# Performance work log

Hardware: AMD Instinct MI355X
Metric: run time of the kernel (lower is better)

Reference implementation:

```python
import jax, jax.numpy as jnp
import numpy as np

ORDER = 4


def setup_inputs() -> dict:
    key = jax.random.key(0)
    k1, k2, k3, k4 = jax.random.split(key, 4)
    B, IN, OUT = 8192, 1024, 1024
    x = jax.random.normal(k1, (B, IN), dtype=jnp.float32)
    base_weight = jax.random.normal(k2, (OUT, IN), dtype=jnp.float32) * (1.0 / np.sqrt(IN))
    std = 1.0 / (IN * np.sqrt(ORDER))
    taylor_coeffs = jax.random.normal(k3, (OUT, IN, ORDER), dtype=jnp.float32) * std
    bound = 1.0 / np.sqrt(IN)
    bias = jax.random.uniform(k4, (OUT,), dtype=jnp.float32, minval=-bound, maxval=bound)
    return {"x": x, "base_weight": base_weight, "taylor_coeffs": taylor_coeffs, "bias": bias}


def reference(x, base_weight, taylor_coeffs, bias):
    # base path: SiLU(x) @ W^T
    base_out = jnp.einsum('bi,oi->bo', jax.nn.silu(x), base_weight)
    # taylor path: x_powers[b,i,k] = x**k, k=0..ORDER-1; contract with coeffs[o,i,k]
    powers = jnp.arange(ORDER, dtype=x.dtype)  # [K]
    x_powers = x[:, :, None] ** powers  # [B, IN, K]
    taylor_out = jnp.einsum('bik,oik->bo', x_powers, taylor_coeffs)
    return base_out + taylor_out + bias
```

## Files before the change

kernel.cpp:

```cpp
#include <hip/hip_runtime.h>
#include <hip/hip_bf16.h>

#define GLOBAL_AS __attribute__((address_space(1)))
#define LDS_AS    __attribute__((address_space(3)))

typedef __bf16 bf16x8 __attribute__((ext_vector_type(8)));
typedef float  f32x4  __attribute__((ext_vector_type(4)));

constexpr int BATCH = 8192;
constexpr int IN    = 1024;
constexpr int OUT   = 1024;
constexpr int KDIM  = IN * 4;
constexpr int BM = 128, BN = 256, BK = 64;
constexpr int NKT  = KDIM / BK;
constexpr int LDSBUF = 24576;

__device__ __forceinline__ unsigned short f2bf(float f) {
    union { float f; unsigned u; } v; v.f = f;
    unsigned r = v.u + 0x7fffu + ((v.u >> 16) & 1u);
    return (unsigned short)(r >> 16);
}
__device__ __forceinline__ unsigned pk(unsigned short a, unsigned short b) {
    return (unsigned)a | ((unsigned)b << 16);
}

__global__ __launch_bounds__(256) void prep_b(const float* __restrict__ W,
                                              const float* __restrict__ C,
                                              const float* __restrict__ bias,
                                              unsigned short* __restrict__ Bb,
                                              float* __restrict__ be) {
    const int o = blockIdx.x, t = threadIdx.x;
    const int i0 = t * 4;
    const float4* c4 = reinterpret_cast<const float4*>(C + ((size_t)o * IN + i0) * 4);
    float4 w4 = *reinterpret_cast<const float4*>(W + (size_t)o * IN + i0);
    float wv[4] = {w4.x, w4.y, w4.z, w4.w};
    float s = 0.f;
    unsigned d[8];
#pragma unroll
    for (int j = 0; j < 4; ++j) {
        float4 c = c4[j];
        s += c.x;
        d[2*j]   = pk(f2bf(wv[j]), f2bf(c.y));
        d[2*j+1] = pk(f2bf(c.z),   f2bf(c.w));
    }
    uint4* dst = reinterpret_cast<uint4*>(Bb + (size_t)o * KDIM + i0 * 4);
    dst[0] = make_uint4(d[0], d[1], d[2], d[3]);
    dst[1] = make_uint4(d[4], d[5], d[6], d[7]);
#pragma unroll
    for (int off = 32; off > 0; off >>= 1) s += __shfl_down(s, off, 64);
    __shared__ float red[4];
    if ((t & 63) == 0) red[t >> 6] = s;
    __syncthreads();
    if (t == 0) be[o] = bias[o] + red[0] + red[1] + red[2] + red[3];
}

__global__ __launch_bounds__(512, 2) void gemm_kan(
        const float* __restrict__ x,
        const unsigned short* __restrict__ Bb,
        const float* __restrict__ be,
        float* __restrict__ out) {
    extern __shared__ unsigned short smem[];

    const int t    = threadIdx.x;
    const int l    = blockIdx.x;
    const int bm   = l & 63;
    const int bn   = l >> 6;
    const int lane = t & 63;
    const int wave = t >> 6;
    const int wr   = wave >> 2;
    const int wc   = wave & 3;
    const int l15  = lane & 15;
    const int quad = lane >> 4;
    const int x7   = l15 & 7;

    const unsigned short* bP[4];
#pragma unroll
    for (int i = 0; i < 4; ++i) {
        int ch = i * 512 + t, r = ch >> 3, g = (ch & 7) ^ (r & 7);
        bP[i] = Bb + (size_t)(bn * BN + r) * KDIM + g * 8;
    }

    const int arow  = t >> 2;
    const int axi   = t & 3;
    const int aoff0 = arow * 64 + (((axi * 2)     ^ (arow & 7)) * 8);
    const int aoff1 = arow * 64 + (((axi * 2 + 1) ^ (arow & 7)) * 8);
    const float4* xp = reinterpret_cast<const float4*>(
        x + (size_t)(bm * BM + arow) * IN + axi * 4);

    const int aRd = (wr * 32 + l15) * 64;
    const int bRd = 8192 + (wc * 64 + l15) * 64;

    f32x4 acc[4][4];
    const f32x4 zero = {0.f, 0.f, 0.f, 0.f};
#pragma unroll
    for (int i = 0; i < 4; ++i)
#pragma unroll
        for (int j = 0; j < 4; ++j) acc[i][j] = zero;

#define STAGE_B(tile, buf) do {                                                        \
    _Pragma("unroll")                                                                  \
    for (int i_ = 0; i_ < 4; ++i_)                                                     \
        __builtin_amdgcn_global_load_lds(                                              \
            (const GLOBAL_AS void*)(bP[i_] + (size_t)(tile) * BK),                     \
            (LDS_AS void*)(smem + (buf) * LDSBUF + 8192 + (i_ * 512 + t) * 8),         \
            16, 0, 0);                                                                 \
} while (0)

#define STAGE_A(buf, v) do {                                                           \
    float e_[4] = {(v).x, (v).y, (v).z, (v).w};                                        \
    unsigned d_[8];                                                                    \
    _Pragma("unroll")                                                                  \
    for (int j = 0; j < 4; ++j) {                                                      \
        float xv_ = e_[j];                                                             \
        float m_  = xv_ * -1.44269504088896f;                          \
        float ex_, r_;                                                                 \
        asm("v_exp_f32 %0, %1" : "=v"(ex_) : "v"(m_));                 \
        float a_  = 1.0f + ex_;                                                        \
        asm("v_rcp_f32 %0, %1" : "=v"(r_) : "v"(a_));                                  \
        float s_  = xv_ * r_;                                                          \
        float x2_ = xv_ * xv_;                                                         \
        float x3_ = x2_ * xv_;                                                         \
        asm("v_cvt_pk_bf16_f32 %0, %1, %2" : "=v"(d_[2*j])   : "v"(s_),  "v"(xv_));    \
        asm("v_cvt_pk_bf16_f32 %0, %1, %2" : "=v"(d_[2*j+1]) : "v"(x2_), "v"(x3_));    \
    }                                                                                  \
    unsigned short* ab_ = smem + (buf) * LDSBUF;                                       \
    *reinterpret_cast<uint4*>(ab_ + aoff0) = make_uint4(d_[0], d_[1], d_[2], d_[3]);   \
    *reinterpret_cast<uint4*>(ab_ + aoff1) = make_uint4(d_[4], d_[5], d_[6], d_[7]);   \
} while (0)

    float4 xa   = xp[0];
    float4 xb   = xp[4];
    float4 xcur = xp[8];
    float4 xnext = xcur;
    STAGE_B(0, 0);
    STAGE_B(1, 1);
    STAGE_A(0, xa);
    STAGE_A(1, xb);
    asm volatile("s_waitcnt vmcnt(4) lgkmcnt(0)" ::: "memory");
    __builtin_amdgcn_s_barrier();

    int cb = 0;
    for (int kt = 0; kt < NKT; ++kt) {
        const unsigned short* sb = smem + cb * LDSBUF;
        const int nb = (cb >= 1) ? cb - 1 : 2;

        if (kt + 3 < NKT) xnext = xp[(kt + 3) * 4];
        if (kt + 2 < NKT) STAGE_B(kt + 2, nb);

#pragma unroll
        for (int kk = 0; kk < 2; ++kk) {
            const int ck = ((kk * 4 + quad) ^ x7) * 8;
            bf16x8 af[4], bv[4];
            af[0] = *reinterpret_cast<const bf16x8*>(sb + aRd + ck);
            af[1] = *reinterpret_cast<const bf16x8*>(sb + aRd + 1024 + ck);
            af[2] = *reinterpret_cast<const bf16x8*>(sb + aRd + 4096 + ck);
            af[3] = *reinterpret_cast<const bf16x8*>(sb + aRd + 5120 + ck);
#pragma unroll
            for (int ni = 0; ni < 4; ++ni)
                bv[ni] = *reinterpret_cast<const bf16x8*>(sb + bRd + ni * 1024 + ck);
#pragma unroll
            for (int mi = 0; mi < 4; ++mi)
#pragma unroll
                for (int ni = 0; ni < 4; ++ni)
                    acc[mi][ni] = __builtin_amdgcn_mfma_f32_16x16x32_bf16(
                        af[mi], bv[ni], acc[mi][ni], 0, 0, 0);
        }

        if (kt + 2 < NKT) {
            STAGE_A(nb, xcur);
            xcur = xnext;
        }

        if (kt < NKT - 3) {
            asm volatile("s_waitcnt vmcnt(5) lgkmcnt(0)" ::: "memory");
            __builtin_amdgcn_s_barrier();
        } else if (kt == NKT - 3) {
            asm volatile("s_waitcnt vmcnt(4) lgkmcnt(0)" ::: "memory");
            __builtin_amdgcn_s_barrier();
        } else if (kt == NKT - 2) {
            asm volatile("s_waitcnt vmcnt(0) lgkmcnt(0)" ::: "memory");
            __builtin_amdgcn_s_barrier();
        }
        cb = (cb == 2) ? 0 : cb + 1;
    }

#undef STAGE_A
#undef STAGE_B

    float bev[4];
#pragma unroll
    for (int ni = 0; ni < 4; ++ni)
        bev[ni] = be[bn * BN + wc * 64 + ni * 16 + l15];

#pragma unroll
    for (int mg = 0; mg < 4; ++mg) {
        const int grow = bm * BM + (mg >> 1) * 64 + wr * 32 + (mg & 1) * 16 + quad * 4;
#pragma unroll
        for (int ni = 0; ni < 4; ++ni) {
            const int gcol = bn * BN + wc * 64 + ni * 16 + l15;
            float* po = out + (size_t)grow * OUT + gcol;
#pragma unroll
            for (int r = 0; r < 4; ++r)
                po[(size_t)r * OUT] = acc[mg][ni][r] + bev[ni];
        }
    }
}

extern "C" void kernel_launch(void* const* d_in, const int* in_sizes, int n_in,
                              void* d_out, int out_size, void* d_ws, size_t ws_size,
                              hipStream_t stream) {
    const float* x    = (const float*)d_in[0];
    const float* W    = (const float*)d_in[1];
    const float* C    = (const float*)d_in[2];
    const float* bias = (const float*)d_in[3];
    float* out = (float*)d_out;

    unsigned short* Bb = (unsigned short*)d_ws;
    float*          be = (float*)(Bb + (size_t)OUT * KDIM);

    constexpr int LDS_BYTES = 3 * LDSBUF * 2;
    static bool inited = false;
    if (!inited) {
        hipFuncSetAttribute(reinterpret_cast<const void*>(&gemm_kan),
                            hipFuncAttributeMaxDynamicSharedMemorySize, LDS_BYTES);
        inited = true;
    }

    prep_b<<<dim3(1024), dim3(256), 0, stream>>>(W, C, bias, Bb, be);

    gemm_kan<<<dim3(256), dim3(512), LDS_BYTES, stream>>>(x, Bb, be, out);
}
```

Baseline: 165.8 us.

## Expand A operand in registers per wave and shrink tile to 128x128

Each wave now loads x directly from global memory in MFMA fragment layout and computes the SiLU and power expansion in registers, so the A tile is no longer staged through LDS. The block tile drops to 128x128 with 256 threads and a 512-block grid, and LDS holds only B. This removes the LDS writes and reads for A and the barrier dependency on them. In exchange, x expansion is repeated by both column waves, x global loads become narrow float2 loads, and B reuse per block is halved.

```diff
diff --git a/kernel.cpp b/kernel.cpp
--- a/kernel.cpp
+++ b/kernel.cpp
@@ -11,9 +11,11 @@
 constexpr int IN    = 1024;
 constexpr int OUT   = 1024;
 constexpr int KDIM  = IN * 4;
-constexpr int BM = 128, BN = 256, BK = 64;
+constexpr int BM = 128, BN = 128, BK = 64;
 constexpr int NKT  = KDIM / BK;
-constexpr int LDSBUF = 24576;
+constexpr int LDSBUF = 8192;
+
+__constant__ int ROWOFF_[4] = {0, 16, 64, 80};
 
 __device__ __forceinline__ unsigned short f2bf(float f) {
     union { float f; unsigned u; } v; v.f = f;
@@ -54,7 +56,7 @@
     if (t == 0) be[o] = bias[o] + red[0] + red[1] + red[2] + red[3];
 }
 
-__global__ __launch_bounds__(512, 2) void gemm_kan(
+__global__ __launch_bounds__(256, 2) void gemm_kan(
         const float* __restrict__ x,
         const unsigned short* __restrict__ Bb,
         const float* __restrict__ be,
@@ -67,8 +69,8 @@
     const int bn   = l >> 6;
     const int lane = t & 63;
     const int wave = t >> 6;
-    const int wr   = wave >> 2;
-    const int wc   = wave & 3;
+    const int wr   = wave >> 1;
+    const int wc   = wave & 1;
     const int l15  = lane & 15;
     const int quad = lane >> 4;
     const int x7   = l15 & 7;
@@ -76,19 +78,13 @@
     const unsigned short* bP[4];
 #pragma unroll
     for (int i = 0; i < 4; ++i) {
-        int ch = i * 512 + t, r = ch >> 3, g = (ch & 7) ^ (r & 7);
+        int ch = i * 256 + t, r = ch >> 3, g = (ch & 7) ^ (r & 7);
         bP[i] = Bb + (size_t)(bn * BN + r) * KDIM + g * 8;
     }
 
-    const int arow  = t >> 2;
-    const int axi   = t & 3;
-    const int aoff0 = arow * 64 + (((axi * 2)     ^ (arow & 7)) * 8);
-    const int aoff1 = arow * 64 + (((axi * 2 + 1) ^ (arow & 7)) * 8);
-    const float4* xp = reinterpret_cast<const float4*>(
-        x + (size_t)(bm * BM + arow) * IN + axi * 4);
-
-    const int aRd = (wr * 32 + l15) * 64;
-    const int bRd = 8192 + (wc * 64 + l15) * 64;
+    const float* xq = x + (size_t)(bm * BM + wr * 32 + l15) * IN + 2 * quad;
+
+    const int bRd = (wc * 64 + l15) * 64;
 
     f32x4 acc[4][4];
     const f32x4 zero = {0.f, 0.f, 0.f, 0.f};
@@ -102,41 +98,43 @@
     for (int i_ = 0; i_ < 4; ++i_)                                                     \
         __builtin_amdgcn_global_load_lds(                                              \
             (const GLOBAL_AS void*)(bP[i_] + (size_t)(tile) * BK),                     \
-            (LDS_AS void*)(smem + (buf) * LDSBUF + 8192 + (i_ * 512 + t) * 8),         \
-            16, 0, 0);                                                                 \
+            (LDS_AS void*)(smem + (buf) * LDSBUF + (i_ * 256 + t) * 8), 16, 0, 0);     \
 } while (0)
 
-#define STAGE_A(buf, v) do {                                                           \
-    float e_[4] = {(v).x, (v).y, (v).z, (v).w};                                        \
-    unsigned d_[8];                                                                    \
+#define XLOAD(dst, tile) do {                                                          \
     _Pragma("unroll")                                                                  \
-    for (int j = 0; j < 4; ++j) {                                                      \
-        float xv_ = e_[j];                                                             \
+    for (int mi_ = 0; mi_ < 4; ++mi_)                                                  \
+        _Pragma("unroll")                                                              \
+        for (int kk_ = 0; kk_ < 2; ++kk_)                                              \
+            (dst)[mi_][kk_] = *reinterpret_cast<const float2*>(                        \
+                xq + (size_t)ROWOFF_[mi_] * IN + (tile) * 16 + kk_ * 8);               \
+} while (0)
+
+#define EXPAND(dst, xv2) do {                                                          \
+    float xa_[2] = {(xv2).x, (xv2).y};                                                 \
+    unsigned u_[4];                                                                    \
+    _Pragma("unroll")                                                                  \
+    for (int e_ = 0; e_ < 2; ++e_) {                                                   \
+        float xv_ = xa_[e_];                                                           \
         float m_  = xv_ * -1.44269504088896f;                          \
         float ex_, r_;                                                                 \
-        asm("v_exp_f32 %0, %1" : "=v"(ex_) : "v"(m_));                 \
+        asm("v_exp_f32 %0, %1" : "=v"(ex_) : "v"(m_));                       \
         float a_  = 1.0f + ex_;                                                        \
         asm("v_rcp_f32 %0, %1" : "=v"(r_) : "v"(a_));                                  \
         float s_  = xv_ * r_;                                                          \
         float x2_ = xv_ * xv_;                                                         \
         float x3_ = x2_ * xv_;                                                         \
-        asm("v_cvt_pk_bf16_f32 %0, %1, %2" : "=v"(d_[2*j])   : "v"(s_),  "v"(xv_));    \
-        asm("v_cvt_pk_bf16_f32 %0, %1, %2" : "=v"(d_[2*j+1]) : "v"(x2_), "v"(x3_));    \
+        asm("v_cvt_pk_bf16_f32 %0, %1, %2" : "=v"(u_[2*e_])   : "v"(s_),  "v"(xv_));   \
+        asm("v_cvt_pk_bf16_f32 %0, %1, %2" : "=v"(u_[2*e_+1]) : "v"(x2_), "v"(x3_));   \
     }                                                                                  \
-    unsigned short* ab_ = smem + (buf) * LDSBUF;                                       \
-    *reinterpret_cast<uint4*>(ab_ + aoff0) = make_uint4(d_[0], d_[1], d_[2], d_[3]);   \
-    *reinterpret_cast<uint4*>(ab_ + aoff1) = make_uint4(d_[4], d_[5], d_[6], d_[7]);   \
+    __builtin_memcpy(&(dst), u_, 16);                                                  \
 } while (0)
 
-    float4 xa   = xp[0];
-    float4 xb   = xp[4];
-    float4 xcur = xp[8];
-    float4 xnext = xcur;
+    float2 xr[4][2];
+    XLOAD(xr, 0);
     STAGE_B(0, 0);
     STAGE_B(1, 1);
-    STAGE_A(0, xa);
-    STAGE_A(1, xb);
-    asm volatile("s_waitcnt vmcnt(4) lgkmcnt(0)" ::: "memory");
+    asm volatile("s_waitcnt vmcnt(4)" ::: "memory");
     __builtin_amdgcn_s_barrier();
 
     int cb = 0;
@@ -144,17 +142,22 @@
         const unsigned short* sb = smem + cb * LDSBUF;
         const int nb = (cb >= 1) ? cb - 1 : 2;
 
-        if (kt + 3 < NKT) xnext = xp[(kt + 3) * 4];
+        float2 xn[4][2];
+        if (kt + 1 < NKT) XLOAD(xn, kt + 1);
+
+        bf16x8 af[2][4];
+#pragma unroll
+        for (int kk = 0; kk < 2; ++kk)
+#pragma unroll
+            for (int mi = 0; mi < 4; ++mi)
+                EXPAND(af[kk][mi], xr[mi][kk]);
+
         if (kt + 2 < NKT) STAGE_B(kt + 2, nb);
 
 #pragma unroll
         for (int kk = 0; kk < 2; ++kk) {
             const int ck = ((kk * 4 + quad) ^ x7) * 8;
-            bf16x8 af[4], bv[4];
-            af[0] = *reinterpret_cast<const bf16x8*>(sb + aRd + ck);
-            af[1] = *reinterpret_cast<const bf16x8*>(sb + aRd + 1024 + ck);
-            af[2] = *reinterpret_cast<const bf16x8*>(sb + aRd + 4096 + ck);
-            af[3] = *reinterpret_cast<const bf16x8*>(sb + aRd + 5120 + ck);
+            bf16x8 bv[4];
 #pragma unroll
             for (int ni = 0; ni < 4; ++ni)
                 bv[ni] = *reinterpret_cast<const bf16x8*>(sb + bRd + ni * 1024 + ck);
@@ -163,29 +166,29 @@
 #pragma unroll
                 for (int ni = 0; ni < 4; ++ni)
                     acc[mi][ni] = __builtin_amdgcn_mfma_f32_16x16x32_bf16(
-                        af[mi], bv[ni], acc[mi][ni], 0, 0, 0);
-        }
-
-        if (kt + 2 < NKT) {
-            STAGE_A(nb, xcur);
-            xcur = xnext;
-        }
-
-        if (kt < NKT - 3) {
-            asm volatile("s_waitcnt vmcnt(5) lgkmcnt(0)" ::: "memory");
-            __builtin_amdgcn_s_barrier();
-        } else if (kt == NKT - 3) {
-            asm volatile("s_waitcnt vmcnt(4) lgkmcnt(0)" ::: "memory");
+                        af[kk][mi], bv[ni], acc[mi][ni], 0, 0, 0);
+        }
+
+        if (kt + 1 < NKT) {
+#pragma unroll
+            for (int mi = 0; mi < 4; ++mi)
+#pragma unroll
+                for (int kk = 0; kk < 2; ++kk) xr[mi][kk] = xn[mi][kk];
+        }
+
+        if (kt < NKT - 2) {
+            asm volatile("s_waitcnt vmcnt(12)" ::: "memory");
             __builtin_amdgcn_s_barrier();
         } else if (kt == NKT - 2) {
-            asm volatile("s_waitcnt vmcnt(0) lgkmcnt(0)" ::: "memory");
+            asm volatile("s_waitcnt vmcnt(8)" ::: "memory");
             __builtin_amdgcn_s_barrier();
         }
         cb = (cb == 2) ? 0 : cb + 1;
     }
 
-#undef STAGE_A
 #undef STAGE_B
+#undef XLOAD
+#undef EXPAND
 
     float bev[4];
 #pragma unroll
@@ -228,5 +231,5 @@
 
     prep_b<<<dim3(1024), dim3(256), 0, stream>>>(W, C, bias, Bb, be);
 
-    gemm_kan<<<dim3(256), dim3(512), LDS_BYTES, stream>>>(x, Bb, be, out);
-}
+    gemm_kan<<<dim3(512), dim3(256), LDS_BYTES, stream>>>(x, Bb, be, out);
+}
```

Result: slower. 224.8 us (+35.6%).
